# Optimization experiments

Measured on AMD Instinct MI355X. Metric: run time of the kernel, lower is better.

The kernel has to match this reference:

```python
import jax, jax.numpy as jnp
import numpy as np

N, DEG, D_IN, D_HID = 50000, 16, 963, 256


def setup_inputs() -> dict:
    key = jax.random.key(0)
    ks = jax.random.split(key, 8)
    s = 0.02
    neighbours = jax.random.randint(ks[0], (N, DEG), 0, N)
    shape_features = jax.random.normal(ks[1], (N, D_IN), dtype=jnp.float32)
    # layer 0: D_IN -> D_HID; layers 1..13 (stacked): D_HID -> D_HID; extra: D_HID -> 3
    W_self0 = jax.random.normal(ks[2], (D_IN, D_HID), dtype=jnp.float32) * s
    W_neigh0 = jax.random.normal(ks[3], (D_IN, D_HID), dtype=jnp.float32) * s
    b0 = jnp.zeros((D_HID,), jnp.float32)
    W_self = jax.random.normal(ks[4], (13, D_HID, D_HID), dtype=jnp.float32) * s
    W_neigh = jax.random.normal(ks[5], (13, D_HID, D_HID), dtype=jnp.float32) * s
    b = jnp.zeros((13, D_HID), jnp.float32)
    W_extra = jax.random.normal(ks[6], (D_HID, 3), dtype=jnp.float32) * s
    b_extra = jnp.zeros((3,), jnp.float32)
    return {
        "neighbours": neighbours,
        "shape_features": shape_features,
        "W_self0": W_self0, "W_neigh0": W_neigh0, "b0": b0,
        "W_self": W_self, "W_neigh": W_neigh, "b": b,
        "W_extra": W_extra, "b_extra": b_extra,
    }


def _gcn(x, neighbours, Ws, Wn, bias):
    # gather neighbour features [N, DEG, D] and sum-aggregate, plus self transform
    agg = jnp.take(x, neighbours, axis=0).sum(axis=1)
    return x @ Ws + agg @ Wn + bias


def reference(neighbours, shape_features, W_self0, W_neigh0, b0, W_self, W_neigh, b, W_extra, b_extra):
    x = jax.nn.relu(_gcn(shape_features, neighbours, W_self0, W_neigh0, b0))
    for i in range(6):  # 6 residual blocks of 2 GCN layers each
        temp = x
        x = jax.nn.relu(_gcn(x, neighbours, W_self[2 * i], W_neigh[2 * i], b[2 * i]))
        x = jax.nn.relu(_gcn(x, neighbours, W_self[2 * i + 1], W_neigh[2 * i + 1], b[2 * i + 1]))
        x = (temp + x) / 2
    x = jax.nn.relu(_gcn(x, neighbours, W_self[12], W_neigh[12], b[12]))
    coordinates = x @ W_extra + b_extra  # extra layer called without neighbours -> linear
    return (x, coordinates)
```

## Files before the change

### kernel.cpp

```cpp
#include <hip/hip_runtime.h>
#include <hip/hip_bf16.h>
#include <hip/hip_fp16.h>
#include <stdint.h>

#define NNODES 50000
#define NPAD   50048
#define DEG    16
#define DIN    963
#define K0PAD  992
#define DHID   256
#define SCALE  (1.0f / 1024.0f)
#define ISCALE 1024.0f

typedef __attribute__((ext_vector_type(4))) float    f32x4;
typedef __attribute__((ext_vector_type(8))) _Float16 f16x8;
typedef __attribute__((ext_vector_type(4))) _Float16 f16x4;

typedef const __attribute__((address_space(1))) void GV;
typedef __attribute__((address_space(3))) void LV;

__device__ __forceinline__ void gl2lds16(const void* g, void* l) {
    __builtin_amdgcn_global_load_lds((GV*)g, (LV*)l, 16, 0, 0);
}

__device__ __forceinline__ int xcd_swz(int bid, int nwg) {
    const int q = nwg >> 3, r_ = nwg & 7, xc = bid & 7;
    return (xc < r_ ? xc * (q + 1) : r_ * (q + 1) + (xc - r_) * q) + (bid >> 3);
}

__global__ __launch_bounds__(256) void gemm_dual0(
    const _Float16* __restrict__ A, int K,
    const _Float16* __restrict__ Wp,
    _Float16* __restrict__ ys, _Float16* __restrict__ yn)
{
    __shared__ _Float16 lds[2][2][4096];

    const int tid  = threadIdx.x;
    const int w    = tid >> 6;
    const int lane = tid & 63;

    const int wgid = xcd_swz(blockIdx.x, gridDim.x);
    const int bm   = (wgid >> 2) << 7;
    const int nb   = (wgid & 3) << 7;

    const int KT = K >> 5;

    auto stage = [&](int s, int kt) {
        const int k0 = kt << 5;
#pragma unroll
        for (int i = 0; i < 2; ++i) {
            const int j   = w + (i << 2);
            const int c   = (j << 6) + lane;
            const int row = c & 127;
            const int k8  = (c >> 7) << 3;
            gl2lds16(A  + (size_t)(bm + row) * K + k0 + k8, &lds[s][0][(size_t)j << 9]);
            gl2lds16(Wp + (size_t)(nb + row) * K + k0 + k8, &lds[s][1][(size_t)j << 9]);
        }
    };

    const int wm = (w >> 1) << 6;
    const int wn = (w & 1) << 6;
    const int lr = lane & 15;
    const int kh = lane >> 4;

    f32x4 acc[4][4] = {};

    stage(0, 0);
    __syncthreads();
    int cur = 0;
    for (int kt = 0; kt < KT; ++kt) {
        if (kt + 1 < KT) stage(cur ^ 1, kt + 1);
        f16x8 a[4], b[4];
#pragma unroll
        for (int mi = 0; mi < 4; ++mi)
            a[mi] = *(const f16x8*)&lds[cur][0][((kh << 7) + wm + (mi << 4) + lr) << 3];
#pragma unroll
        for (int ni = 0; ni < 4; ++ni)
            b[ni] = *(const f16x8*)&lds[cur][1][((kh << 7) + wn + (ni << 4) + lr) << 3];
#pragma unroll
        for (int mi = 0; mi < 4; ++mi)
#pragma unroll
            for (int ni = 0; ni < 4; ++ni)
                acc[mi][ni] = __builtin_amdgcn_mfma_f32_16x16x32_f16(b[ni], a[mi], acc[mi][ni], 0, 0, 0);
        __syncthreads();
        cur ^= 1;
    }

    _Float16* C = (nb < 256) ? ys : yn;
    const int cb = (nb & 255) + wn;
#pragma unroll
    for (int mi = 0; mi < 4; ++mi) {
        const int m = bm + wm + (mi << 4) + lr;
#pragma unroll
        for (int ni = 0; ni < 4; ++ni) {
            const int col0 = cb + (ni << 4) + (kh << 2);
            f16x4 o;
#pragma unroll
            for (int r = 0; r < 4; ++r) o[r] = (_Float16)acc[mi][ni][r];
            *(f16x4*)(C + ((size_t)m << 8) + col0) = o;
        }
    }
}

template<int FINAL>
__global__ __launch_bounds__(512) void fused_layer(
    const _Float16* __restrict__ X, const int* __restrict__ nbr,
    const _Float16* __restrict__ W, const float* __restrict__ bias,
    const _Float16* __restrict__ res,
    _Float16* __restrict__ outh, float* __restrict__ outf)
{
    __shared__ _Float16 ldsA[2][4096];
    __shared__ _Float16 ldsB[2][8192];

    const int tid  = threadIdx.x;
    const int w    = tid >> 6;
    const int lane = tid & 63;
    const int bm   = blockIdx.x << 7;

    const int growg = bm + (tid >> 2);
    const int nrow  = (growg < NNODES) ? growg : (NNODES - 1);
    const int4* np  = (const int4*)(nbr + nrow * DEG);
    const int4 q0 = np[0], q1 = np[1], q2 = np[2], q3 = np[3];
    const int kq = (tid & 3) << 3;

    auto GLD = [&](int r, int ko) -> f16x8 {
        return *(const f16x8*)(X + ((size_t)r << 8) + ko);
    };
    auto stageAself = [&](int s, int kt) {
        const int c = tid;
        gl2lds16(X + ((size_t)(bm + (c & 127)) << 8) + (kt << 5) + ((c >> 7) << 3),
                 &ldsA[s][(size_t)c << 3]);
    };
    auto stageB = [&](int s, int kt) {
#pragma unroll
        for (int i = 0; i < 2; ++i) {
            const int c = (i << 9) + tid;
            gl2lds16(W + ((size_t)(c & 255) << 9) + (kt << 5) + ((c >> 8) << 3),
                     &ldsB[s][(size_t)c << 3]);
        }
    };

    const int wm = (w >> 2) << 6;
    const int wn = (w & 3) << 6;
    const int lr = lane & 15;
    const int kh = lane >> 4;

    f32x4 acc[4][4] = {};
    f16x8 g0, g1, g2, g3, g4, g5, g6, g7;

    stageAself(0, 0);
    stageB(0, 0);
    __syncthreads();

    int cur = 0;
#pragma unroll
    for (int kt = 0; kt < 16; ++kt) {
        const int nxt = kt + 1;
        if (nxt < 16) {
            if (nxt < 8) {
                stageAself(cur ^ 1, nxt);
            } else {
                const int ko = ((nxt - 8) << 5) + kq;
                g0 = GLD(q0.x, ko); g1 = GLD(q0.y, ko); g2 = GLD(q0.z, ko); g3 = GLD(q0.w, ko);
                g4 = GLD(q1.x, ko); g5 = GLD(q1.y, ko); g6 = GLD(q1.z, ko); g7 = GLD(q1.w, ko);
            }
            stageB(cur ^ 1, nxt);
        }
        f16x8 a[4], b[4];
#pragma unroll
        for (int mi = 0; mi < 4; ++mi)
            a[mi] = *(const f16x8*)&ldsA[cur][((kh << 7) + wm + (mi << 4) + lr) << 3];
#pragma unroll
        for (int ni = 0; ni < 4; ++ni)
            b[ni] = *(const f16x8*)&ldsB[cur][((kh << 8) + wn + (ni << 4) + lr) << 3];
#pragma unroll
        for (int mi = 0; mi < 4; ++mi)
#pragma unroll
            for (int ni = 0; ni < 4; ++ni)
                acc[mi][ni] = __builtin_amdgcn_mfma_f32_16x16x32_f16(b[ni], a[mi], acc[mi][ni], 0, 0, 0);
        if (nxt >= 8 && nxt < 16) {
            const int ko = ((nxt - 8) << 5) + kq;
            f16x8 s0 = ((g0 + g1) + (g2 + g3)) + ((g4 + g5) + (g6 + g7));
            g0 = GLD(q2.x, ko); g1 = GLD(q2.y, ko); g2 = GLD(q2.z, ko); g3 = GLD(q2.w, ko);
            g4 = GLD(q3.x, ko); g5 = GLD(q3.y, ko); g6 = GLD(q3.z, ko); g7 = GLD(q3.w, ko);
            f16x8 s1 = ((g0 + g1) + (g2 + g3)) + ((g4 + g5) + (g6 + g7));
            *(f16x8*)&ldsA[cur ^ 1][(size_t)(((tid & 3) << 7) + (tid >> 2)) << 3] = s0 + s1;
        }
        __syncthreads();
        cur ^= 1;
    }

#pragma unroll
    for (int mi = 0; mi < 4; ++mi) {
        const int m = bm + wm + (mi << 4) + lr;
        const size_t mb = (size_t)m << 8;
#pragma unroll
        for (int ni = 0; ni < 4; ++ni) {
            const int col0 = wn + (ni << 4) + (kh << 2);
            const float4 bv = *(const float4*)(bias + col0);
            float s0 = fmaxf(acc[mi][ni][0] + bv.x * SCALE, 0.f);
            float s1 = fmaxf(acc[mi][ni][1] + bv.y * SCALE, 0.f);
            float s2 = fmaxf(acc[mi][ni][2] + bv.z * SCALE, 0.f);
            float s3 = fmaxf(acc[mi][ni][3] + bv.w * SCALE, 0.f);
            if (res) {
                const f16x4 rv = *(const f16x4*)(res + mb + col0);
                s0 = ((float)rv[0] + s0) * 0.5f;
                s1 = ((float)rv[1] + s1) * 0.5f;
                s2 = ((float)rv[2] + s2) * 0.5f;
                s3 = ((float)rv[3] + s3) * 0.5f;
            }
            if (FINAL) {
                if (m < NNODES) {
                    float4 o = make_float4(s0 * ISCALE, s1 * ISCALE, s2 * ISCALE, s3 * ISCALE);
                    *(float4*)(outf + mb + col0) = o;
                }
            } else {
                f16x4 o;
                o[0] = (_Float16)s0; o[1] = (_Float16)s1;
                o[2] = (_Float16)s2; o[3] = (_Float16)s3;
                *(f16x4*)(outh + mb + col0) = o;
            }
        }
    }
}

__global__ __launch_bounds__(256) void combine16(
    const _Float16* __restrict__ ys, const _Float16* __restrict__ yn,
    const int* __restrict__ nbr, const float* __restrict__ bias,
    _Float16* __restrict__ outh)
{
    const int idx = blockIdx.x * 256 + threadIdx.x;
    const int r   = idx >> 5;
    const int c8  = (idx & 31) << 3;
    const int4* np = (const int4*)(nbr + r * DEG);
    const int4 q0 = np[0], q1 = np[1], q2 = np[2], q3 = np[3];

    f16x8 v[16];
#define LD16(slot, n) v[slot] = *(const f16x8*)(yn + ((size_t)(n) << 8) + c8)
    LD16(0,  q0.x); LD16(1,  q0.y); LD16(2,  q0.z); LD16(3,  q0.w);
    LD16(4,  q1.x); LD16(5,  q1.y); LD16(6,  q1.z); LD16(7,  q1.w);
    LD16(8,  q2.x); LD16(9,  q2.y); LD16(10, q2.z); LD16(11, q2.w);
    LD16(12, q3.x); LD16(13, q3.y); LD16(14, q3.z); LD16(15, q3.w);
#undef LD16
    const f16x8 ysv = *(const f16x8*)(ys + ((size_t)r << 8) + c8);
    const float4 b0 = *(const float4*)(bias + c8);
    const float4 b1 = *(const float4*)(bias + c8 + 4);
    const float bb[8] = {b0.x, b0.y, b0.z, b0.w, b1.x, b1.y, b1.z, b1.w};
    f16x8 o;
#pragma unroll
    for (int i = 0; i < 8; ++i) {
        float s = (float)ysv[i] + bb[i] * SCALE;
#pragma unroll
        for (int j = 0; j < 16; ++j) s += (float)v[j][i];
        o[i] = (_Float16)fmaxf(s, 0.f);
    }
    *(f16x8*)(outh + ((size_t)r << 8) + c8) = o;
}

__global__ __launch_bounds__(64) void coords_kernel(
    const float* __restrict__ x, const float* __restrict__ We,
    const float* __restrict__ be, float* __restrict__ out3, int N)
{
    const int n = blockIdx.x;
    const int l = threadIdx.x;
    const float4 xv = *(const float4*)(x + (size_t)n * 256 + l * 4);
    float p0 = 0.f, p1 = 0.f, p2 = 0.f;
    const float xs[4] = {xv.x, xv.y, xv.z, xv.w};
#pragma unroll
    for (int i = 0; i < 4; ++i) {
        const int cidx = l * 4 + i;
        p0 += xs[i] * We[cidx * 3 + 0];
        p1 += xs[i] * We[cidx * 3 + 1];
        p2 += xs[i] * We[cidx * 3 + 2];
    }
#pragma unroll
    for (int off = 32; off > 0; off >>= 1) {
        p0 += __shfl_down(p0, off);
        p1 += __shfl_down(p1, off);
        p2 += __shfl_down(p2, off);
    }
    if (l == 0) {
        out3[(size_t)n * 3 + 0] = p0 + be[0];
        out3[(size_t)n * 3 + 1] = p1 + be[1];
        out3[(size_t)n * 3 + 2] = p2 + be[2];
    }
}

__global__ __launch_bounds__(256) void conv_sf(const float* __restrict__ sf,
                                               _Float16* __restrict__ sfb)
{
    const int idx = blockIdx.x * 256 + threadIdx.x;
    const int row = idx / 124;
    const int k8  = (idx % 124) << 3;
    f16x8 o = {};
    if (row < NNODES) {
#pragma unroll
        for (int i = 0; i < 8; ++i) {
            const int k = k8 + i;
            o[i] = (k < DIN) ? (_Float16)(sf[(size_t)row * DIN + k] * SCALE) : (_Float16)0.f;
        }
    }
    *(f16x8*)(sfb + (size_t)row * K0PAD + k8) = o;
}

__global__ __launch_bounds__(256) void pack_w0(const float* __restrict__ Ws0,
                                               const float* __restrict__ Wn0,
                                               _Float16* __restrict__ Wp0)
{
    const int idx = blockIdx.x * 256 + threadIdx.x;
    const int nn  = idx & 511;
    const int k8  = idx >> 9;
    const float* W = (nn < 256) ? Ws0 : Wn0;
    const int n0 = nn & 255;
    f16x8 o;
#pragma unroll
    for (int i = 0; i < 8; ++i) {
        const int k = (k8 << 3) + i;
        o[i] = (k < DIN) ? (_Float16)W[(size_t)k * 256 + n0] : (_Float16)0.f;
    }
    *(f16x8*)(Wp0 + (size_t)nn * K0PAD + (k8 << 3)) = o;
}

__global__ __launch_bounds__(256) void pack_w2(const float* __restrict__ Ws,
                                               const float* __restrict__ Wn,
                                               _Float16* __restrict__ Wpk2)
{
    const int idx = blockIdx.x * 256 + threadIdx.x;
    const int n   = idx & 255;
    const int k8  = (idx >> 8) & 63;
    const int l   = idx >> 14;
    f16x8 o;
#pragma unroll
    for (int i = 0; i < 8; ++i) {
        const int k = (k8 << 3) + i;
        const float* W = (k < 256) ? Ws : Wn;
        o[i] = (_Float16)W[(size_t)l * 65536 + (k & 255) * 256 + n];
    }
    *(f16x8*)(Wpk2 + (size_t)l * 131072 + (size_t)n * 512 + (k8 << 3)) = o;
}

extern "C" void kernel_launch(void* const* d_in, const int* in_sizes, int n_in,
                              void* d_out, int out_size, void* d_ws, size_t ws_size,
                              hipStream_t stream)
{
    const int*   nbr = (const int*)d_in[0];
    const float* sf  = (const float*)d_in[1];
    const float* Ws0 = (const float*)d_in[2];
    const float* Wn0 = (const float*)d_in[3];
    const float* b0  = (const float*)d_in[4];
    const float* Ws  = (const float*)d_in[5];
    const float* Wn  = (const float*)d_in[6];
    const float* bb  = (const float*)d_in[7];
    const float* We  = (const float*)d_in[8];
    const float* be  = (const float*)d_in[9];
    float* out = (float*)d_out;

    uint8_t* w = (uint8_t*)d_ws;
    _Float16* sfb  = (_Float16*)w;
    _Float16* P    = (_Float16*)w;
    _Float16* Q    = P + (size_t)NPAD * 256;
    _Float16* Wpk2 = Q + (size_t)NPAD * 256;
    _Float16* Wp0  = (_Float16*)(w + (size_t)NPAD * K0PAD * 2);
    _Float16* ysb  = Wp0 + (size_t)512 * K0PAD;
    _Float16* ynb  = ysb + (size_t)NPAD * 256;

    conv_sf<<<NPAD * 124 / 256, 256, 0, stream>>>(sf, sfb);
    pack_w0<<<512 * 124 / 256, 256, 0, stream>>>(Ws0, Wn0, Wp0);

    gemm_dual0<<<(NPAD / 128) * 4, 256, 0, stream>>>(sfb, K0PAD, Wp0, ysb, ynb);
    pack_w2<<<13 * 64 * 256 / 256, 256, 0, stream>>>(Ws, Wn, Wpk2);
    combine16<<<NNODES * 32 / 256, 256, 0, stream>>>(ysb, ynb, nbr, b0, P);

    const int fg = NPAD / 128;

    for (int t = 0; t < 6; ++t) {
        const int lA = 2 * t, lB = lA + 1;
        fused_layer<0><<<fg, 512, 0, stream>>>(P, nbr, Wpk2 + (size_t)lA * 131072,
                                               bb + lA * 256, nullptr, Q, nullptr);
        fused_layer<0><<<fg, 512, 0, stream>>>(Q, nbr, Wpk2 + (size_t)lB * 131072,
                                               bb + lB * 256, P, P, nullptr);
    }

    fused_layer<1><<<fg, 512, 0, stream>>>(P, nbr, Wpk2 + (size_t)12 * 131072,
                                           bb + 12 * 256, nullptr, nullptr, out);

    coords_kernel<<<NNODES, 64, 0, stream>>>(out, We, be, out + (size_t)NNODES * 256, NNODES);
}
```

Measured before the change: 1.546 ms.

## Precompute neighbour aggregation into LDS before the GEMM K-loop

```diff
diff --git a/kernel.cpp b/kernel.cpp
--- a/kernel.cpp
+++ b/kernel.cpp
@@ -109,6 +109,7 @@
     const _Float16* __restrict__ res,
     _Float16* __restrict__ outh, float* __restrict__ outf)
 {
+    __shared__ _Float16 ldsAgg[8][4096];
     __shared__ _Float16 ldsA[2][4096];
     __shared__ _Float16 ldsB[2][8192];
 
@@ -117,15 +118,6 @@
     const int lane = tid & 63;
     const int bm   = blockIdx.x << 7;
 
-    const int growg = bm + (tid >> 2);
-    const int nrow  = (growg < NNODES) ? growg : (NNODES - 1);
-    const int4* np  = (const int4*)(nbr + nrow * DEG);
-    const int4 q0 = np[0], q1 = np[1], q2 = np[2], q3 = np[3];
-    const int kq = (tid & 3) << 3;
-
-    auto GLD = [&](int r, int ko) -> f16x8 {
-        return *(const f16x8*)(X + ((size_t)r << 8) + ko);
-    };
     auto stageAself = [&](int s, int kt) {
         const int c = tid;
         gl2lds16(X + ((size_t)(bm + (c & 127)) << 8) + (kt << 5) + ((c >> 7) << 3),
@@ -140,36 +132,63 @@
         }
     };
 
+    stageAself(0, 0);
+    stageB(0, 0);
+
+    {
+        const int row  = tid >> 2;
+        const int sl   = tid & 3;
+        const int grow = bm + row;
+        const int nrow = (grow < NNODES) ? grow : (NNODES - 1);
+        const int4* np = (const int4*)(nbr + nrow * DEG);
+        const int4 q0 = np[0], q1 = np[1], q2 = np[2], q3 = np[3];
+        const _Float16* xb = X + (sl << 6);
+
+        f16x8 p0[8], p1[8], v[8];
+#define GLD8(NB, DST) { const _Float16* b_ = xb + ((size_t)(NB) << 8); \
+        _Pragma("unroll") for (int c = 0; c < 8; ++c) DST[c] = *(const f16x8*)(b_ + (c << 3)); }
+#define ACC8(NB, P) { GLD8(NB, v); _Pragma("unroll") for (int c = 0; c < 8; ++c) P[c] += v[c]; }
+        GLD8(q0.x, p0); GLD8(q0.y, p1);
+        ACC8(q0.z, p0); ACC8(q0.w, p1);
+        ACC8(q1.x, p0); ACC8(q1.y, p1);
+        ACC8(q1.z, p0); ACC8(q1.w, p1);
+        ACC8(q2.x, p0); ACC8(q2.y, p1);
+        ACC8(q2.z, p0); ACC8(q2.w, p1);
+        ACC8(q3.x, p0); ACC8(q3.y, p1);
+        ACC8(q3.z, p0); ACC8(q3.w, p1);
+#undef ACC8
+#undef GLD8
+#pragma unroll
+        for (int c = 0; c < 8; ++c) {
+            const f16x8 s = p0[c] + p1[c];
+            *(f16x8*)&ldsAgg[(sl << 1) + (c >> 2)][(((c & 3) << 7) + row) << 3] = s;
+        }
+    }
+    __syncthreads();
+
     const int wm = (w >> 2) << 6;
     const int wn = (w & 3) << 6;
     const int lr = lane & 15;
     const int kh = lane >> 4;
 
     f32x4 acc[4][4] = {};
-    f16x8 g0, g1, g2, g3, g4, g5, g6, g7;
-
-    stageAself(0, 0);
-    stageB(0, 0);
-    __syncthreads();
 
     int cur = 0;
 #pragma unroll
     for (int kt = 0; kt < 16; ++kt) {
         const int nxt = kt + 1;
-        if (nxt < 16) {
-            if (nxt < 8) {
-                stageAself(cur ^ 1, nxt);
-            } else {
-                const int ko = ((nxt - 8) << 5) + kq;
-                g0 = GLD(q0.x, ko); g1 = GLD(q0.y, ko); g2 = GLD(q0.z, ko); g3 = GLD(q0.w, ko);
-                g4 = GLD(q1.x, ko); g5 = GLD(q1.y, ko); g6 = GLD(q1.z, ko); g7 = GLD(q1.w, ko);
-            }
-            stageB(cur ^ 1, nxt);
-        }
+        if (nxt < 8)  stageAself(cur ^ 1, nxt);
+        if (nxt < 16) stageB(cur ^ 1, nxt);
         f16x8 a[4], b[4];
-#pragma unroll
-        for (int mi = 0; mi < 4; ++mi)
-            a[mi] = *(const f16x8*)&ldsA[cur][((kh << 7) + wm + (mi << 4) + lr) << 3];
+        if (kt < 8) {
+#pragma unroll
+            for (int mi = 0; mi < 4; ++mi)
+                a[mi] = *(const f16x8*)&ldsA[cur][((kh << 7) + wm + (mi << 4) + lr) << 3];
+        } else {
+#pragma unroll
+            for (int mi = 0; mi < 4; ++mi)
+                a[mi] = *(const f16x8*)&ldsAgg[kt - 8][((kh << 7) + wm + (mi << 4) + lr) << 3];
+        }
 #pragma unroll
         for (int ni = 0; ni < 4; ++ni)
             b[ni] = *(const f16x8*)&ldsB[cur][((kh << 8) + wn + (ni << 4) + lr) << 3];
@@ -178,14 +197,6 @@
 #pragma unroll
             for (int ni = 0; ni < 4; ++ni)
                 acc[mi][ni] = __builtin_amdgcn_mfma_f32_16x16x32_f16(b[ni], a[mi], acc[mi][ni], 0, 0, 0);
-        if (nxt >= 8 && nxt < 16) {
-            const int ko = ((nxt - 8) << 5) + kq;
-            f16x8 s0 = ((g0 + g1) + (g2 + g3)) + ((g4 + g5) + (g6 + g7));
-            g0 = GLD(q2.x, ko); g1 = GLD(q2.y, ko); g2 = GLD(q2.z, ko); g3 = GLD(q2.w, ko);
-            g4 = GLD(q3.x, ko); g5 = GLD(q3.y, ko); g6 = GLD(q3.z, ko); g7 = GLD(q3.w, ko);
-            f16x8 s1 = ((g0 + g1) + (g2 + g3)) + ((g4 + g5) + (g6 + g7));
-            *(f16x8*)&ldsA[cur ^ 1][(size_t)(((tid & 3) << 7) + (tid >> 2)) << 3] = s0 + s1;
-        }
         __syncthreads();
         cur ^= 1;
     }
```

Result: slower. 2.034 ms (+31.5%).

## Shrink fused layer tile to 64 rows and load weights directly into registers

Applied to the files above, without the earlier changes.

```diff
diff --git a/kernel.cpp b/kernel.cpp
--- a/kernel.cpp
+++ b/kernel.cpp
@@ -103,19 +103,20 @@
 }
 
 template<int FINAL>
-__global__ __launch_bounds__(512) void fused_layer(
+__global__ __launch_bounds__(256) void fused64(
     const _Float16* __restrict__ X, const int* __restrict__ nbr,
     const _Float16* __restrict__ W, const float* __restrict__ bias,
     const _Float16* __restrict__ res,
     _Float16* __restrict__ outh, float* __restrict__ outf)
 {
-    __shared__ _Float16 ldsA[2][4096];
-    __shared__ _Float16 ldsB[2][8192];
+    __shared__ _Float16 ldsA[2][2048];
 
     const int tid  = threadIdx.x;
     const int w    = tid >> 6;
     const int lane = tid & 63;
-    const int bm   = blockIdx.x << 7;
+
+    const int wgid = xcd_swz(blockIdx.x, gridDim.x);
+    const int bm   = wgid << 6;
 
     const int growg = bm + (tid >> 2);
     const int nrow  = (growg < NNODES) ? growg : (NNODES - 1);
@@ -128,34 +129,33 @@
     };
     auto stageAself = [&](int s, int kt) {
         const int c = tid;
-        gl2lds16(X + ((size_t)(bm + (c & 127)) << 8) + (kt << 5) + ((c >> 7) << 3),
+        gl2lds16(X + ((size_t)(bm + (c & 63)) << 8) + (kt << 5) + ((c >> 6) << 3),
                  &ldsA[s][(size_t)c << 3]);
     };
-    auto stageB = [&](int s, int kt) {
-#pragma unroll
-        for (int i = 0; i < 2; ++i) {
-            const int c = (i << 9) + tid;
-            gl2lds16(W + ((size_t)(c & 255) << 9) + (kt << 5) + ((c >> 8) << 3),
-                     &ldsB[s][(size_t)c << 3]);
-        }
-    };
-
-    const int wm = (w >> 2) << 6;
-    const int wn = (w & 3) << 6;
+
+    const int wn = w << 6;
     const int lr = lane & 15;
     const int kh = lane >> 4;
 
+    const _Float16* Wb = W + ((size_t)(wn + lr) << 9) + (kh << 3);
+    auto LDB = [&](int ni, int kt) -> f16x8 {
+        return *(const f16x8*)(Wb + ((size_t)ni << 13) + (kt << 5));
+    };
+
     f32x4 acc[4][4] = {};
     f16x8 g0, g1, g2, g3, g4, g5, g6, g7;
 
     stageAself(0, 0);
-    stageB(0, 0);
+    f16x8 bc[4];
+#pragma unroll
+    for (int ni = 0; ni < 4; ++ni) bc[ni] = LDB(ni, 0);
     __syncthreads();
 
     int cur = 0;
 #pragma unroll
     for (int kt = 0; kt < 16; ++kt) {
         const int nxt = kt + 1;
+        f16x8 bn[4];
         if (nxt < 16) {
             if (nxt < 8) {
                 stageAself(cur ^ 1, nxt);
@@ -164,35 +164,37 @@
                 g0 = GLD(q0.x, ko); g1 = GLD(q0.y, ko); g2 = GLD(q0.z, ko); g3 = GLD(q0.w, ko);
                 g4 = GLD(q1.x, ko); g5 = GLD(q1.y, ko); g6 = GLD(q1.z, ko); g7 = GLD(q1.w, ko);
             }
-            stageB(cur ^ 1, nxt);
-        }
-        f16x8 a[4], b[4];
+#pragma unroll
+            for (int ni = 0; ni < 4; ++ni) bn[ni] = LDB(ni, nxt);
+        }
+        f16x8 a[4];
 #pragma unroll
         for (int mi = 0; mi < 4; ++mi)
-            a[mi] = *(const f16x8*)&ldsA[cur][((kh << 7) + wm + (mi << 4) + lr) << 3];
-#pragma unroll
-        for (int ni = 0; ni < 4; ++ni)
-            b[ni] = *(const f16x8*)&ldsB[cur][((kh << 8) + wn + (ni << 4) + lr) << 3];
+            a[mi] = *(const f16x8*)&ldsA[cur][((kh << 6) + (mi << 4) + lr) << 3];
 #pragma unroll
         for (int mi = 0; mi < 4; ++mi)
 #pragma unroll
             for (int ni = 0; ni < 4; ++ni)
-                acc[mi][ni] = __builtin_amdgcn_mfma_f32_16x16x32_f16(b[ni], a[mi], acc[mi][ni], 0, 0, 0);
+                acc[mi][ni] = __builtin_amdgcn_mfma_f32_16x16x32_f16(bc[ni], a[mi], acc[mi][ni], 0, 0, 0);
         if (nxt >= 8 && nxt < 16) {
             const int ko = ((nxt - 8) << 5) + kq;
             f16x8 s0 = ((g0 + g1) + (g2 + g3)) + ((g4 + g5) + (g6 + g7));
             g0 = GLD(q2.x, ko); g1 = GLD(q2.y, ko); g2 = GLD(q2.z, ko); g3 = GLD(q2.w, ko);
             g4 = GLD(q3.x, ko); g5 = GLD(q3.y, ko); g6 = GLD(q3.z, ko); g7 = GLD(q3.w, ko);
             f16x8 s1 = ((g0 + g1) + (g2 + g3)) + ((g4 + g5) + (g6 + g7));
-            *(f16x8*)&ldsA[cur ^ 1][(size_t)(((tid & 3) << 7) + (tid >> 2)) << 3] = s0 + s1;
+            *(f16x8*)&ldsA[cur ^ 1][(size_t)(((tid & 3) << 9) + ((tid >> 2) << 3))] = s0 + s1;
         }
         __syncthreads();
+        if (nxt < 16) {
+#pragma unroll
+            for (int ni = 0; ni < 4; ++ni) bc[ni] = bn[ni];
+        }
         cur ^= 1;
     }
 
 #pragma unroll
     for (int mi = 0; mi < 4; ++mi) {
-        const int m = bm + wm + (mi << 4) + lr;
+        const int m = bm + (mi << 4) + lr;
         const size_t mb = (size_t)m << 8;
 #pragma unroll
         for (int ni = 0; ni < 4; ++ni) {
@@ -371,18 +373,18 @@
     pack_w2<<<13 * 64 * 256 / 256, 256, 0, stream>>>(Ws, Wn, Wpk2);
     combine16<<<NNODES * 32 / 256, 256, 0, stream>>>(ysb, ynb, nbr, b0, P);
 
-    const int fg = NPAD / 128;
+    const int fg = NPAD / 64;
 
     for (int t = 0; t < 6; ++t) {
         const int lA = 2 * t, lB = lA + 1;
-        fused_layer<0><<<fg, 512, 0, stream>>>(P, nbr, Wpk2 + (size_t)lA * 131072,
-                                               bb + lA * 256, nullptr, Q, nullptr);
-        fused_layer<0><<<fg, 512, 0, stream>>>(Q, nbr, Wpk2 + (size_t)lB * 131072,
-                                               bb + lB * 256, P, P, nullptr);
-    }
-
-    fused_layer<1><<<fg, 512, 0, stream>>>(P, nbr, Wpk2 + (size_t)12 * 131072,
-                                           bb + 12 * 256, nullptr, nullptr, out);
+        fused64<0><<<fg, 256, 0, stream>>>(P, nbr, Wpk2 + (size_t)lA * 131072,
+                                           bb + lA * 256, nullptr, Q, nullptr);
+        fused64<0><<<fg, 256, 0, stream>>>(Q, nbr, Wpk2 + (size_t)lB * 131072,
+                                           bb + lB * 256, P, P, nullptr);
+    }
+
+    fused64<1><<<fg, 256, 0, stream>>>(P, nbr, Wpk2 + (size_t)12 * 131072,
+                                       bb + 12 * 256, nullptr, nullptr, out);
 
     coords_kernel<<<NNODES, 64, 0, stream>>>(out, We, be, out + (size_t)NNODES * 256, NNODES);
 }
```

Measured after the change: 1.548 ms. Within noise of the previous version (+0.1%).
